# Kernel tuning notes

Hardware: AMD Instinct MI355X
Metric: run time of the kernel (lower is better)

The kernel has to match this reference:

```python
import jax, jax.numpy as jnp
import numpy as np

B, S, D = 2, 1024, 5120
NH, NKV, HD = 80, 8, 128
GROUPS = NH // NKV
SCALE = HD ** -0.5
ROPE_THETA = 1.0e7


def setup_inputs() -> dict:
    key = jax.random.key(0)
    ks = jax.random.split(key, 8)
    hidden_states = jax.random.normal(ks[0], (B, S, D), dtype=jnp.float32)
    # real RoPE tables from rope_theta (default rope_type)
    inv_freq = 1.0 / (ROPE_THETA ** (np.arange(0, HD, 2, dtype=np.float32) / HD))  # [HD/2]
    pos = np.arange(S, dtype=np.float32)
    freqs = np.outer(pos, inv_freq)                      # [S, HD/2]
    emb = np.concatenate([freqs, freqs], axis=-1)        # [S, HD]
    cos = jnp.asarray(np.broadcast_to(np.cos(emb), (B, S, HD)).copy())
    sin = jnp.asarray(np.broadcast_to(np.sin(emb), (B, S, HD)).copy())
    w_scale = 0.02
    q_w = jax.random.normal(ks[1], (NH * HD, D), dtype=jnp.float32) * w_scale
    q_b = jax.random.normal(ks[2], (NH * HD,), dtype=jnp.float32) * w_scale
    k_w = jax.random.normal(ks[3], (NKV * HD, D), dtype=jnp.float32) * w_scale
    k_b = jax.random.normal(ks[4], (NKV * HD,), dtype=jnp.float32) * w_scale
    v_w = jax.random.normal(ks[5], (NKV * HD, D), dtype=jnp.float32) * w_scale
    v_b = jax.random.normal(ks[6], (NKV * HD,), dtype=jnp.float32) * w_scale
    o_w = jax.random.normal(ks[7], (D, NH * HD), dtype=jnp.float32) * w_scale
    return dict(hidden_states=hidden_states, cos=cos, sin=sin,
                q_w=q_w, q_b=q_b, k_w=k_w, k_b=k_b, v_w=v_w, v_b=v_b, o_w=o_w)


def _rotate_half(x):
    x1, x2 = jnp.split(x, 2, axis=-1)
    return jnp.concatenate([-x2, x1], axis=-1)


def reference(hidden_states, cos, sin, q_w, q_b, k_w, k_b, v_w, v_b, o_w):
    b, s, _ = hidden_states.shape
    # QKV projections (bias on q/k/v per attention_bias=True)
    q = (hidden_states @ q_w.T + q_b).reshape(b, s, NH, HD).transpose(0, 2, 1, 3)   # [b,NH,s,hd]
    k = (hidden_states @ k_w.T + k_b).reshape(b, s, NKV, HD).transpose(0, 2, 1, 3)  # [b,NKV,s,hd]
    v = (hidden_states @ v_w.T + v_b).reshape(b, s, NKV, HD).transpose(0, 2, 1, 3)
    # RoPE (rotate_half form); cos/sin broadcast over head dim
    c = cos[:, None, :, :]
    sn = sin[:, None, :, :]
    q = q * c + _rotate_half(q) * sn
    k = k * c + _rotate_half(k) * sn
    # GQA: repeat kv heads to match query heads
    k = jnp.repeat(k, GROUPS, axis=1)  # [b,NH,s,hd]
    v = jnp.repeat(v, GROUPS, axis=1)
    scores = jnp.einsum('bhqd,bhkd->bhqk', q, k) * SCALE
    causal = jnp.tril(jnp.ones((s, s), dtype=bool))
    scores = jnp.where(causal[None, None], scores, jnp.finfo(scores.dtype).min)
    attn = jax.nn.softmax(scores, axis=-1)
    out = jnp.einsum('bhqk,bhkd->bhqd', attn, v)                 # [b,NH,s,hd]
    out = out.transpose(0, 2, 1, 3).reshape(b, s, NH * HD)
    return out @ o_w.T                                           # o_proj, no bias
```

## Files before the change

### kernel.cpp

```cpp
#include <hip/hip_runtime.h>
#include <hip/hip_bf16.h>

#define NH 80
#define NKV 8
#define HD 128
#define GROUPS 10
#define SEQ 1024
#define BATCH 2
#define DMODEL 5120
#define NQKV 12288
#define MROWS 2048
#define QCOLS 10240
#define KOFF 10240
#define VOFF 11264
#define ATTN_SCALE 0.08838834764831845f

typedef __attribute__((ext_vector_type(8))) __bf16 bf16x8;
typedef __attribute__((ext_vector_type(4))) float f32x4;

__device__ inline unsigned short f2bf(float f) {
  unsigned u = __float_as_uint(f);
  u = (u + 0x7fffu + ((u >> 16) & 1u)) >> 16;
  return (unsigned short)u;
}
__device__ inline float bf2f(unsigned short h) {
  return __uint_as_float(((unsigned)h) << 16);
}

template <typename T>
__device__ inline T ld_vec(const void* p) {
  T v;
  __builtin_memcpy(&v, p, sizeof(T));
  return v;
}

__device__ inline void gload_lds16(const void* g, void* l) {
  __builtin_amdgcn_global_load_lds(
      (const __attribute__((address_space(1))) void*)g,
      (__attribute__((address_space(3))) void*)l, 16, 0, 0);
}

__global__ __launch_bounds__(256) void cvt_all(
    const float* __restrict__ hs, const float* __restrict__ qw,
    const float* __restrict__ kw, const float* __restrict__ vw,
    const float* __restrict__ ow, unsigned short* __restrict__ wsd) {
  long i8 = (long)blockIdx.x * 256 + threadIdx.x;
  const float* src;
  unsigned short* dst;
  long so;
  if (i8 < 1310720)      { src = hs; so = i8;           dst = wsd; }
  else if (i8 < 7864320) { src = qw; so = i8 - 1310720; dst = wsd + 10485760; }
  else if (i8 < 8519680) { src = kw; so = i8 - 7864320; dst = wsd + 62914560; }
  else if (i8 < 9175040) { src = vw; so = i8 - 8519680; dst = wsd + 68157440; }
  else                   { src = ow; so = i8 - 9175040; dst = wsd + 73400320; }
  long e = so * 8;
  float4 a = *reinterpret_cast<const float4*>(src + e);
  float4 b = *reinterpret_cast<const float4*>(src + e + 4);
  union { unsigned short u[8]; uint4 v; } r;
  r.u[0] = f2bf(a.x); r.u[1] = f2bf(a.y); r.u[2] = f2bf(a.z); r.u[3] = f2bf(a.w);
  r.u[4] = f2bf(b.x); r.u[5] = f2bf(b.y); r.u[6] = f2bf(b.z); r.u[7] = f2bf(b.w);
  *reinterpret_cast<uint4*>(dst + e) = r.v;
}

__global__ __launch_bounds__(256) void concat_bias(
    const float* __restrict__ qb, const float* __restrict__ kb,
    const float* __restrict__ vb, float* __restrict__ out) {
  int i = blockIdx.x * 256 + threadIdx.x;
  if (i >= NQKV) return;
  float v;
  if (i < KOFF) v = qb[i];
  else if (i < VOFF) v = kb[i - KOFF];
  else v = vb[i - VOFF];
  out[i] = v;
}

template <int OUT_BF16, int HAS_BIAS>
__global__ __launch_bounds__(256, 4) void gemm_bt64(
    const unsigned short* __restrict__ A, const unsigned short* __restrict__ W,
    const float* __restrict__ bias, void* __restrict__ Cout,
    int M, int N, int K) {
  __shared__ unsigned short As[128 * 64];
  __shared__ unsigned short Bs[128 * 64];
  const int t = threadIdx.x;
  const int lane = t & 63, wave = t >> 6;
  const int m0 = blockIdx.y * 128, n0 = blockIdx.x * 128;
  const int wr = (wave >> 1) * 64, wc = (wave & 1) * 64;
  const int lr = lane & 15, lg = lane >> 4;
  int st_row[4], st_col[4];
#pragma unroll
  for (int ch = 0; ch < 4; ++ch) {
    int ol = wave * 1024 + ch * 4096 + lane * 16;
    int row = ol >> 7, cb = ol & 127;
    st_row[ch] = row;
    st_col[ch] = cb ^ ((row & 7) << 4);
  }
  f32x4 acc[4][4] = {};
  const int swz = (lr & 7) << 4;
  for (int k0 = 0; k0 < K; k0 += 64) {
#pragma unroll
    for (int ch = 0; ch < 4; ++ch) {
      int od = wave * 1024 + ch * 4096;
      gload_lds16((const char*)A +
                      ((size_t)(m0 + st_row[ch]) * K + k0) * 2 + st_col[ch],
                  (char*)As + od);
      gload_lds16((const char*)W +
                      ((size_t)(n0 + st_row[ch]) * K + k0) * 2 + st_col[ch],
                  (char*)Bs + od);
    }
    __syncthreads();
    bf16x8 af[4][2], bfr[4][2];
#pragma unroll
    for (int ks = 0; ks < 2; ++ks) {
      int colb = (ks * 64 + lg * 16) ^ swz;
#pragma unroll
      for (int m = 0; m < 4; ++m)
        af[m][ks] =
            ld_vec<bf16x8>((const char*)As + (wr + m * 16 + lr) * 128 + colb);
#pragma unroll
      for (int n = 0; n < 4; ++n)
        bfr[n][ks] =
            ld_vec<bf16x8>((const char*)Bs + (wc + n * 16 + lr) * 128 + colb);
    }
#pragma unroll
    for (int ks = 0; ks < 2; ++ks)
#pragma unroll
      for (int m = 0; m < 4; ++m)
#pragma unroll
        for (int n = 0; n < 4; ++n)
          acc[m][n] = __builtin_amdgcn_mfma_f32_16x16x32_bf16(
              af[m][ks], bfr[n][ks], acc[m][n], 0, 0, 0);
    __syncthreads();
  }
#pragma unroll
  for (int n = 0; n < 4; ++n) {
    int col = n0 + wc + n * 16 + lr;
    float bv = HAS_BIAS ? bias[col] : 0.0f;
#pragma unroll
    for (int m = 0; m < 4; ++m) {
#pragma unroll
      for (int r = 0; r < 4; ++r) {
        int row = m0 + wr + m * 16 + lg * 4 + r;
        float v = acc[m][n][r] + bv;
        if (OUT_BF16)
          ((unsigned short*)Cout)[(size_t)row * N + col] = f2bf(v);
        else
          ((float*)Cout)[(size_t)row * N + col] = v;
      }
    }
  }
}

__global__ __launch_bounds__(256) void rope_kernel(
    unsigned short* __restrict__ qkv, const float* __restrict__ cs,
    const float* __restrict__ sn) {
  int idx = blockIdx.x * 256 + threadIdx.x;
  int quad = idx & 15;
  int rest = idx >> 4;
  int slot = rest % 88;
  int row = rest / 88;
  if (row >= MROWS) return;
  int col = slot < NH ? slot * HD : KOFF + (slot - NH) * HD;
  unsigned short* p = qkv + (size_t)row * NQKV + col;
  const float* cp = cs + (size_t)row * HD;
  const float* sp = sn + (size_t)row * HD;
  int d0 = quad * 4;
  float4 c1 = *reinterpret_cast<const float4*>(cp + d0);
  float4 s1 = *reinterpret_cast<const float4*>(sp + d0);
  float4 c2 = *reinterpret_cast<const float4*>(cp + d0 + 64);
  float4 s2 = *reinterpret_cast<const float4*>(sp + d0 + 64);
  ushort4 x1 = *reinterpret_cast<const ushort4*>(p + d0);
  ushort4 x2 = *reinterpret_cast<const ushort4*>(p + d0 + 64);
  ushort4 o1, o2;
  float a, b;
  a = bf2f(x1.x); b = bf2f(x2.x);
  o1.x = f2bf(a * c1.x - b * s1.x); o2.x = f2bf(b * c2.x + a * s2.x);
  a = bf2f(x1.y); b = bf2f(x2.y);
  o1.y = f2bf(a * c1.y - b * s1.y); o2.y = f2bf(b * c2.y + a * s2.y);
  a = bf2f(x1.z); b = bf2f(x2.z);
  o1.z = f2bf(a * c1.z - b * s1.z); o2.z = f2bf(b * c2.z + a * s2.z);
  a = bf2f(x1.w); b = bf2f(x2.w);
  o1.w = f2bf(a * c1.w - b * s1.w); o2.w = f2bf(b * c2.w + a * s2.w);
  *reinterpret_cast<ushort4*>(p + d0) = o1;
  *reinterpret_cast<ushort4*>(p + d0 + 64) = o2;
}

__global__ __launch_bounds__(256, 2) void attn_kernel(
    const unsigned short* __restrict__ qkv, unsigned short* __restrict__ out) {
  __shared__ unsigned short Ks[64][128];
  __shared__ unsigned short Vt[128][64];
  __shared__ unsigned short Ps[4][32][72];
  const int t = threadIdx.x, lane = t & 63, wave = t >> 6;
  const int lr = lane & 15, lg = lane >> 4;
  const int blk = blockIdx.x;
  const int qt = 7 - blk / 160;
  const int bh = blk % 160;
  const int h = bh % NH, b = bh / NH;
  const int kvh = h / GROUPS;
  const int q0 = qt * 128;
  const int wrow0 = q0 + wave * 32;
  const unsigned short* Qb = qkv + (size_t)(b * SEQ) * NQKV + h * HD;
  const unsigned short* Kb = qkv + (size_t)(b * SEQ) * NQKV + KOFF + kvh * HD;
  const unsigned short* Vb = qkv + (size_t)(b * SEQ) * NQKV + VOFF + kvh * HD;
  int kst_row[4], kst_col[4];
#pragma unroll
  for (int ch = 0; ch < 4; ++ch) {
    int ol = wave * 1024 + ch * 4096 + lane * 16;
    int row = ol >> 8, cbyte = ol & 255;
    kst_row[ch] = row;
    kst_col[ch] = cbyte ^ ((row & 7) << 4);
  }
  bf16x8 qf[2][4];
#pragma unroll
  for (int rb = 0; rb < 2; ++rb)
#pragma unroll
    for (int kk = 0; kk < 4; ++kk)
      qf[rb][kk] = ld_vec<bf16x8>(Qb + (size_t)(wrow0 + rb * 16 + lr) * NQKV +
                                  kk * 32 + lg * 8);
  f32x4 acc[2][8] = {};
  float mrow[2][4], lrow[2][4];
#pragma unroll
  for (int rb = 0; rb < 2; ++rb)
#pragma unroll
    for (int r = 0; r < 4; ++r) { mrow[rb][r] = -__builtin_inff(); lrow[rb][r] = 0.f; }

  const int ntile = (q0 + 128) >> 6;
  for (int tt = 0; tt < ntile; ++tt) {
    const int kv0 = tt * 64;
    __syncthreads();
#pragma unroll
    for (int ch = 0; ch < 4; ++ch) {
      int od = wave * 1024 + ch * 4096;
      gload_lds16((const char*)Kb + ((size_t)(kv0 + kst_row[ch]) * NQKV) * 2 +
                      kst_col[ch],
                  (char*)&Ks[0][0] + od);
    }
#pragma unroll
    for (int i = 0; i < 4; ++i) {
      int e = i * 2048 + t * 8;
      int row = e >> 7, colc = e & 127;
      uint4 dv = ld_vec<uint4>(Vb + (size_t)(kv0 + row) * NQKV + colc);
      const unsigned short* pv = reinterpret_cast<const unsigned short*>(&dv);
#pragma unroll
      for (int j = 0; j < 8; ++j) {
        int dd = colc + j;
        int gp = ((row >> 3) + dd + (dd >> 3)) & 7;
        Vt[dd][(gp << 3) | (row & 7)] = pv[j];
      }
    }
    __syncthreads();
    if (kv0 > wrow0 + 31) continue;
    const bool needMask = (kv0 + 63) > wrow0;
#pragma unroll
    for (int rb = 0; rb < 2; ++rb) {
      f32x4 sf[4] = {};
#pragma unroll
      for (int kk = 0; kk < 4; ++kk) {
#pragma unroll
        for (int cb = 0; cb < 4; ++cb) {
          bf16x8 kfr = ld_vec<bf16x8>(
              (const char*)&Ks[0][0] + (cb * 16 + lr) * 256 +
              ((kk * 64 + lg * 16) ^ ((lr & 7) << 4)));
          sf[cb] = __builtin_amdgcn_mfma_f32_16x16x32_bf16(qf[rb][kk], kfr,
                                                           sf[cb], 0, 0, 0);
        }
      }
#pragma unroll
      for (int r = 0; r < 4; ++r) {
        int qrow = wrow0 + rb * 16 + lg * 4 + r;
        float mx = -3.0e38f;
#pragma unroll
        for (int cb = 0; cb < 4; ++cb) {
          float s = sf[cb][r] * ATTN_SCALE;
          if (needMask && (kv0 + cb * 16 + lr) > qrow) s = -__builtin_inff();
          sf[cb][r] = s;
          mx = fmaxf(mx, s);
        }
        mx = fmaxf(mx, __shfl_xor(mx, 1));
        mx = fmaxf(mx, __shfl_xor(mx, 2));
        mx = fmaxf(mx, __shfl_xor(mx, 4));
        mx = fmaxf(mx, __shfl_xor(mx, 8));
        float mold = mrow[rb][r];
        float mnew = fmaxf(mold, mx);
        float sfac = __expf(mold - mnew);
        mrow[rb][r] = mnew;
        float ps = 0.f;
#pragma unroll
        for (int cb = 0; cb < 4; ++cb) {
          float p = __expf(sf[cb][r] - mnew);
          ps += p;
          Ps[wave][rb * 16 + lg * 4 + r][cb * 16 + lr] = f2bf(p);
        }
        ps += __shfl_xor(ps, 1);
        ps += __shfl_xor(ps, 2);
        ps += __shfl_xor(ps, 4);
        ps += __shfl_xor(ps, 8);
        lrow[rb][r] = lrow[rb][r] * sfac + ps;
#pragma unroll
        for (int n = 0; n < 8; ++n) acc[rb][n][r] *= sfac;
      }
    }
#pragma unroll
    for (int kk = 0; kk < 2; ++kk) {
      bf16x8 vf[8];
#pragma unroll
      for (int cb = 0; cb < 8; ++cb) {
        int dd = cb * 16 + lr;
        int gp = (kk * 4 + lg + dd + (dd >> 3)) & 7;
        vf[cb] = ld_vec<bf16x8>(&Vt[dd][gp << 3]);
      }
#pragma unroll
      for (int rb = 0; rb < 2; ++rb) {
        bf16x8 pa = ld_vec<bf16x8>(&Ps[wave][rb * 16 + lr][kk * 32 + lg * 8]);
#pragma unroll
        for (int cb = 0; cb < 8; ++cb)
          acc[rb][cb] = __builtin_amdgcn_mfma_f32_16x16x32_bf16(pa, vf[cb],
                                                                acc[rb][cb], 0, 0, 0);
      }
    }
  }
#pragma unroll
  for (int rb = 0; rb < 2; ++rb)
#pragma unroll
    for (int n = 0; n < 8; ++n)
#pragma unroll
      for (int r = 0; r < 4; ++r) {
        int qrow = wrow0 + rb * 16 + lg * 4 + r;
        float v = acc[rb][n][r] / lrow[rb][r];
        out[(size_t)(b * SEQ + qrow) * QCOLS + h * HD + n * 16 + lr] = f2bf(v);
      }
}

extern "C" void kernel_launch(void* const* d_in, const int* in_sizes, int n_in,
                              void* d_out, int out_size, void* d_ws,
                              size_t ws_size, hipStream_t stream) {
  const float* hs   = (const float*)d_in[0];
  const float* cosb = (const float*)d_in[1];
  const float* sinb = (const float*)d_in[2];
  const float* q_w  = (const float*)d_in[3];
  const float* q_b  = (const float*)d_in[4];
  const float* k_w  = (const float*)d_in[5];
  const float* k_b  = (const float*)d_in[6];
  const float* v_w  = (const float*)d_in[7];
  const float* v_b  = (const float*)d_in[8];
  const float* o_w  = (const float*)d_in[9];

  char* ws = (char*)d_ws;
  unsigned short* hsB  = (unsigned short*)(ws);
  unsigned short* wqkv = (unsigned short*)(ws + 20971520ll);
  unsigned short* wo   = (unsigned short*)(ws + 146800640ll);
  unsigned short* qkv  = (unsigned short*)(ws + 251658240ll);
  unsigned short* attn = (unsigned short*)(ws + 301989888ll);
  float* bqkv          = (float*)(ws + 343932928ll);

  cvt_all<<<dim3(61440), dim3(256), 0, stream>>>(hs, q_w, k_w, v_w, o_w,
                                                 (unsigned short*)ws);
  concat_bias<<<dim3(48), dim3(256), 0, stream>>>(q_b, k_b, v_b, bqkv);

  gemm_bt64<1, 1><<<dim3(96, 16), dim3(256), 0, stream>>>(
      hsB, wqkv, bqkv, qkv, MROWS, NQKV, DMODEL);
  rope_kernel<<<dim3(11264), dim3(256), 0, stream>>>(qkv, cosb, sinb);
  attn_kernel<<<dim3(1280), dim3(256), 0, stream>>>(qkv, attn);
  gemm_bt64<0, 0><<<dim3(40, 16), dim3(256), 0, stream>>>(
      attn, wo, nullptr, d_out, MROWS, 5120, 10240);
}
```

Before: 793.5 us.

## Double-buffer GEMM LDS tiles with K=32 stages to overlap loads and MFMA

Replaces the single-buffer K=64 GEMM loop with a two-stage ping-pong pipeline over K=32 slices. The next slice's global-to-LDS copy is issued before computing on the current buffer, so memory latency can hide behind MFMA work. It adds a manual vmcnt wait, barrier and sched_barrier fence, plus a new swizzle for the 64-byte rows. Launch bounds drop from 4 to 2 blocks per CU, which trades occupancy for the in-block overlap.

```diff
diff --git a/kernel.cpp b/kernel.cpp
--- a/kernel.cpp
+++ b/kernel.cpp
@@ -75,61 +75,73 @@
 }
 
 template <int OUT_BF16, int HAS_BIAS>
-__global__ __launch_bounds__(256, 4) void gemm_bt64(
+__global__ __launch_bounds__(256, 2) void gemm_db32(
     const unsigned short* __restrict__ A, const unsigned short* __restrict__ W,
     const float* __restrict__ bias, void* __restrict__ Cout,
     int M, int N, int K) {
-  __shared__ unsigned short As[128 * 64];
-  __shared__ unsigned short Bs[128 * 64];
+  __shared__ unsigned short As[2][128 * 32];
+  __shared__ unsigned short Bs[2][128 * 32];
   const int t = threadIdx.x;
   const int lane = t & 63, wave = t >> 6;
   const int m0 = blockIdx.y * 128, n0 = blockIdx.x * 128;
   const int wr = (wave >> 1) * 64, wc = (wave & 1) * 64;
   const int lr = lane & 15, lg = lane >> 4;
-  int st_row[4], st_col[4];
-#pragma unroll
-  for (int ch = 0; ch < 4; ++ch) {
-    int ol = wave * 1024 + ch * 4096 + lane * 16;
-    int row = ol >> 7, cb = ol & 127;
-    st_row[ch] = row;
-    st_col[ch] = cb ^ ((row & 7) << 4);
+  int st_row[2], st_col[2];
+#pragma unroll
+  for (int ch = 0; ch < 2; ++ch) {
+    int o = ch * 4096 + wave * 1024 + lane * 16;
+    int u = o ^ (((o >> 7) & 7) << 4);
+    st_row[ch] = u >> 6;
+    st_col[ch] = u & 63;
   }
   f32x4 acc[4][4] = {};
-  const int swz = (lr & 7) << 4;
-  for (int k0 = 0; k0 < K; k0 += 64) {
-#pragma unroll
-    for (int ch = 0; ch < 4; ++ch) {
-      int od = wave * 1024 + ch * 4096;
+  const int swzl = ((lr >> 1) & 7) << 4;
+  auto STAGE = [&](int buf, int k0) {
+#pragma unroll
+    for (int ch = 0; ch < 2; ++ch) {
+      int od = ch * 4096 + wave * 1024;
       gload_lds16((const char*)A +
                       ((size_t)(m0 + st_row[ch]) * K + k0) * 2 + st_col[ch],
-                  (char*)As + od);
+                  (char*)&As[buf][0] + od);
       gload_lds16((const char*)W +
                       ((size_t)(n0 + st_row[ch]) * K + k0) * 2 + st_col[ch],
-                  (char*)Bs + od);
-    }
-    __syncthreads();
-    bf16x8 af[4][2], bfr[4][2];
-#pragma unroll
-    for (int ks = 0; ks < 2; ++ks) {
-      int colb = (ks * 64 + lg * 16) ^ swz;
-#pragma unroll
-      for (int m = 0; m < 4; ++m)
-        af[m][ks] =
-            ld_vec<bf16x8>((const char*)As + (wr + m * 16 + lr) * 128 + colb);
+                  (char*)&Bs[buf][0] + od);
+    }
+  };
+  auto COMPUTE = [&](int buf) {
+    bf16x8 af[4], bfr[4];
+#pragma unroll
+    for (int m = 0; m < 4; ++m) {
+      int o = (wr + m * 16 + lr) * 64 + lg * 16;
+      af[m] = ld_vec<bf16x8>((const char*)&As[buf][0] + (o ^ swzl));
+    }
+#pragma unroll
+    for (int n = 0; n < 4; ++n) {
+      int o = (wc + n * 16 + lr) * 64 + lg * 16;
+      bfr[n] = ld_vec<bf16x8>((const char*)&Bs[buf][0] + (o ^ swzl));
+    }
+#pragma unroll
+    for (int m = 0; m < 4; ++m)
 #pragma unroll
       for (int n = 0; n < 4; ++n)
-        bfr[n][ks] =
-            ld_vec<bf16x8>((const char*)Bs + (wc + n * 16 + lr) * 128 + colb);
-    }
-#pragma unroll
-    for (int ks = 0; ks < 2; ++ks)
-#pragma unroll
-      for (int m = 0; m < 4; ++m)
-#pragma unroll
-        for (int n = 0; n < 4; ++n)
-          acc[m][n] = __builtin_amdgcn_mfma_f32_16x16x32_bf16(
-              af[m][ks], bfr[n][ks], acc[m][n], 0, 0, 0);
-    __syncthreads();
+        acc[m][n] = __builtin_amdgcn_mfma_f32_16x16x32_bf16(af[m], bfr[n],
+                                                            acc[m][n], 0, 0, 0);
+  };
+  auto FENCE = [&]() {
+    asm volatile("s_waitcnt vmcnt(0)" ::: "memory");
+    __builtin_amdgcn_s_barrier();
+    __builtin_amdgcn_sched_barrier(0);
+  };
+
+  STAGE(0, 0);
+  __syncthreads();
+  for (int k0 = 0; k0 < K; k0 += 64) {
+    STAGE(1, k0 + 32);
+    COMPUTE(0);
+    FENCE();
+    if (k0 + 64 < K) STAGE(0, k0 + 64);
+    COMPUTE(1);
+    FENCE();
   }
 #pragma unroll
   for (int n = 0; n < 4; ++n) {
@@ -356,10 +368,10 @@
                                                  (unsigned short*)ws);
   concat_bias<<<dim3(48), dim3(256), 0, stream>>>(q_b, k_b, v_b, bqkv);
 
-  gemm_bt64<1, 1><<<dim3(96, 16), dim3(256), 0, stream>>>(
+  gemm_db32<1, 1><<<dim3(96, 16), dim3(256), 0, stream>>>(
       hsB, wqkv, bqkv, qkv, MROWS, NQKV, DMODEL);
   rope_kernel<<<dim3(11264), dim3(256), 0, stream>>>(qkv, cosb, sinb);
   attn_kernel<<<dim3(1280), dim3(256), 0, stream>>>(qkv, attn);
-  gemm_bt64<0, 0><<<dim3(40, 16), dim3(256), 0, stream>>>(
+  gemm_db32<0, 0><<<dim3(40, 16), dim3(256), 0, stream>>>(
       attn, wo, nullptr, d_out, MROWS, 5120, 10240);
 }
```

After: 927.8 us. 16.9% more time.

## Split-K the output projection with atomic accumulation and fuse bias concat into conversion

Applied to the files above, without the earlier changes.

The o_proj GEMM is split into two K halves launched along grid z, each accumulating into a zeroed output via float atomicAdd, so the launch covers more blocks than the CUs can hold at once. The bias concatenation is folded into the conversion kernel as extra threads, removing one launch. The trade is an added memset of the output, atomic read-modify-write traffic, and non-deterministic summation order.

```diff
diff --git a/kernel.cpp b/kernel.cpp
--- a/kernel.cpp
+++ b/kernel.cpp
@@ -43,8 +43,23 @@
 __global__ __launch_bounds__(256) void cvt_all(
     const float* __restrict__ hs, const float* __restrict__ qw,
     const float* __restrict__ kw, const float* __restrict__ vw,
-    const float* __restrict__ ow, unsigned short* __restrict__ wsd) {
+    const float* __restrict__ ow, unsigned short* __restrict__ wsd,
+    const float* __restrict__ qb, const float* __restrict__ kb,
+    const float* __restrict__ vb, float* __restrict__ bqkv) {
   long i8 = (long)blockIdx.x * 256 + threadIdx.x;
+  if (i8 >= 15728640) {
+    long e = (i8 - 15728640) * 8;
+    const float* src;
+    long o;
+    if (e < 10240)      { src = qb; o = e; }
+    else if (e < 11264) { src = kb; o = e - 10240; }
+    else                { src = vb; o = e - 11264; }
+    float4 a = *reinterpret_cast<const float4*>(src + o);
+    float4 b = *reinterpret_cast<const float4*>(src + o + 4);
+    *reinterpret_cast<float4*>(bqkv + e) = a;
+    *reinterpret_cast<float4*>(bqkv + e + 4) = b;
+    return;
+  }
   const float* src;
   unsigned short* dst;
   long so;
@@ -62,28 +77,19 @@
   *reinterpret_cast<uint4*>(dst + e) = r.v;
 }
 
-__global__ __launch_bounds__(256) void concat_bias(
-    const float* __restrict__ qb, const float* __restrict__ kb,
-    const float* __restrict__ vb, float* __restrict__ out) {
-  int i = blockIdx.x * 256 + threadIdx.x;
-  if (i >= NQKV) return;
-  float v;
-  if (i < KOFF) v = qb[i];
-  else if (i < VOFF) v = kb[i - KOFF];
-  else v = vb[i - VOFF];
-  out[i] = v;
-}
-
-template <int OUT_BF16, int HAS_BIAS>
+template <int OUT_BF16, int HAS_BIAS, int ATOMIC_OUT>
 __global__ __launch_bounds__(256, 4) void gemm_bt64(
     const unsigned short* __restrict__ A, const unsigned short* __restrict__ W,
     const float* __restrict__ bias, void* __restrict__ Cout,
-    int M, int N, int K) {
+    int M, int N, int K, int LDA) {
   __shared__ unsigned short As[128 * 64];
   __shared__ unsigned short Bs[128 * 64];
   const int t = threadIdx.x;
   const int lane = t & 63, wave = t >> 6;
   const int m0 = blockIdx.y * 128, n0 = blockIdx.x * 128;
+  const size_t kofs = (size_t)blockIdx.z * K;
+  const unsigned short* Ab = A + kofs;
+  const unsigned short* Wb = W + kofs;
   const int wr = (wave >> 1) * 64, wc = (wave & 1) * 64;
   const int lr = lane & 15, lg = lane >> 4;
   int st_row[4], st_col[4];
@@ -100,11 +106,11 @@
 #pragma unroll
     for (int ch = 0; ch < 4; ++ch) {
       int od = wave * 1024 + ch * 4096;
-      gload_lds16((const char*)A +
-                      ((size_t)(m0 + st_row[ch]) * K + k0) * 2 + st_col[ch],
+      gload_lds16((const char*)Ab +
+                      ((size_t)(m0 + st_row[ch]) * LDA + k0) * 2 + st_col[ch],
                   (char*)As + od);
-      gload_lds16((const char*)W +
-                      ((size_t)(n0 + st_row[ch]) * K + k0) * 2 + st_col[ch],
+      gload_lds16((const char*)Wb +
+                      ((size_t)(n0 + st_row[ch]) * LDA + k0) * 2 + st_col[ch],
                   (char*)Bs + od);
     }
     __syncthreads();
@@ -141,10 +147,13 @@
       for (int r = 0; r < 4; ++r) {
         int row = m0 + wr + m * 16 + lg * 4 + r;
         float v = acc[m][n][r] + bv;
-        if (OUT_BF16)
+        if (OUT_BF16) {
           ((unsigned short*)Cout)[(size_t)row * N + col] = f2bf(v);
-        else
+        } else if (ATOMIC_OUT) {
+          atomicAdd((float*)Cout + (size_t)row * N + col, v);
+        } else {
           ((float*)Cout)[(size_t)row * N + col] = v;
+        }
       }
     }
   }
@@ -352,14 +361,15 @@
   unsigned short* attn = (unsigned short*)(ws + 301989888ll);
   float* bqkv          = (float*)(ws + 343932928ll);
 
-  cvt_all<<<dim3(61440), dim3(256), 0, stream>>>(hs, q_w, k_w, v_w, o_w,
-                                                 (unsigned short*)ws);
-  concat_bias<<<dim3(48), dim3(256), 0, stream>>>(q_b, k_b, v_b, bqkv);
-
-  gemm_bt64<1, 1><<<dim3(96, 16), dim3(256), 0, stream>>>(
-      hsB, wqkv, bqkv, qkv, MROWS, NQKV, DMODEL);
+  cvt_all<<<dim3(61446), dim3(256), 0, stream>>>(
+      hs, q_w, k_w, v_w, o_w, (unsigned short*)ws, q_b, k_b, v_b, bqkv);
+
+  gemm_bt64<1, 1, 0><<<dim3(96, 16, 1), dim3(256), 0, stream>>>(
+      hsB, wqkv, bqkv, qkv, MROWS, NQKV, DMODEL, DMODEL);
   rope_kernel<<<dim3(11264), dim3(256), 0, stream>>>(qkv, cosb, sinb);
   attn_kernel<<<dim3(1280), dim3(256), 0, stream>>>(qkv, attn);
-  gemm_bt64<0, 0><<<dim3(40, 16), dim3(256), 0, stream>>>(
-      attn, wo, nullptr, d_out, MROWS, 5120, 10240);
-}
+
+  hipMemsetAsync(d_out, 0, (size_t)MROWS * 5120 * sizeof(float), stream);
+  gemm_bt64<0, 0, 1><<<dim3(40, 16, 2), dim3(256), 0, stream>>>(
+      attn, wo, nullptr, d_out, MROWS, 5120, 5120, 10240);
+}
```

Result: slower. 831.5 us (+4.8%).
